# Performance work log

Hardware: AMD Instinct MI355X
Metric: run time of the kernel (lower is better)

Reference implementation:

```python
import jax, jax.numpy as jnp
import numpy as np

B, S, D, H, L, FF, V, TYPES = 16, 512, 1024, 16, 8, 4096, 30522, 2
DH = D // H
BETA = 1.0          # pbit_temperature
EPS = 1e-12         # layer_norm_eps
STD = 0.02          # initializer_range


def _ln(x, g, b):
    m = x.mean(-1, keepdims=True)
    v = ((x - m) ** 2).mean(-1, keepdims=True)
    return (x - m) * jax.lax.rsqrt(v + EPS) * g + b


def setup_inputs() -> dict:
    key = jax.random.key(0)
    ks = iter(jax.random.split(key, 32))
    rn = lambda shape: (jax.random.normal(next(ks), shape, dtype=jnp.float32) * STD)
    inp = {
        'input_ids': jax.random.randint(next(ks), (B, S), 0, V),
        'token_type_ids': jax.random.randint(next(ks), (B, S), 0, TYPES),
        'tok_emb': rn((V, D)),
        'pos_emb': rn((S, D)),
        'type_emb': rn((TYPES, D)),
        'emb_g': jnp.ones((D,), jnp.float32),
        'emb_b': jnp.zeros((D,), jnp.float32),
        # stacked per-layer parameters [L, ...]
        'Wq': rn((L, D, D)), 'bq': jnp.zeros((L, D), jnp.float32),
        'Wk': rn((L, D, D)), 'bk': jnp.zeros((L, D), jnp.float32),
        'Wv': rn((L, D, D)), 'bv': jnp.zeros((L, D), jnp.float32),
        'Wo': rn((L, D, D)), 'bo': jnp.zeros((L, D), jnp.float32),
        'ln1_g': jnp.ones((L, D), jnp.float32), 'ln1_b': jnp.zeros((L, D), jnp.float32),
        'ln2_g': jnp.ones((L, D), jnp.float32), 'ln2_b': jnp.zeros((L, D), jnp.float32),
        'W1': rn((L, D, FF)), 'b1': jnp.zeros((L, FF), jnp.float32),
        'W2': rn((L, FF, D)), 'b2': jnp.zeros((L, D), jnp.float32),
    }
    return inp


def reference(input_ids, token_type_ids, tok_emb, pos_emb, type_emb, emb_g, emb_b,
              Wq, bq, Wk, bk, Wv, bv, Wo, bo, ln1_g, ln1_b, ln2_g, ln2_b,
              W1, b1, W2, b2):
    # Embeddings (eval mode: TSU noise + dropout are identity)
    h = tok_emb[input_ids] + pos_emb[None, :, :] + type_emb[token_type_ids]
    h = _ln(h, emb_g, emb_b)

    def layer(h, p):
        wq, bq_, wk, bk_, wv, bv_, wo, bo_, g1, bb1, g2, bb2, w1, bf1, w2, bf2 = p
        x = _ln(h, g1, bb1)  # pre-LN per TinyBioBERTLayer
        q = (x @ wq + bq_).reshape(B, S, H, DH)
        k = (x @ wk + bk_).reshape(B, S, H, DH)
        v = (x @ wv + bv_).reshape(B, S, H, DH)
        # P-bit attention in expectation == temperature-scaled softmax SDPA
        scores = jnp.einsum('bqhd,bkhd->bhqk', q, k) * (BETA / np.sqrt(DH))
        a = jax.nn.softmax(scores, axis=-1)
        ctx = jnp.einsum('bhqk,bkhd->bqhd', a, v).reshape(B, S, D)
        h = h + ctx @ wo + bo_
        y = _ln(h, g2, bb2)
        y = jax.nn.gelu(y @ w1 + bf1, approximate=False) @ w2 + bf2
        return h + y, None

    params = (Wq, bq, Wk, bk, Wv, bv, Wo, bo, ln1_g, ln1_b, ln2_g, ln2_b, W1, b1, W2, b2)
    h, _ = jax.lax.scan(layer, h, params)
    return h
```

## Files before the change

### kernel.cpp

```cpp
#include <hip/hip_runtime.h>
#include <math.h>

#define B_  16
#define S_  512
#define D_  1024
#define H_  16
#define DH_ 64
#define L_  8
#define FF_ 4096
#define M_  (B_*S_)

typedef __attribute__((ext_vector_type(4))) float  f32x4;
typedef __attribute__((ext_vector_type(8))) short  s8v;
typedef __attribute__((ext_vector_type(4))) short  s4v;
typedef __attribute__((ext_vector_type(8))) __bf16 bf8v;

__device__ __forceinline__ short f2bf(float f) {
  union { float f; unsigned u; } x; x.f = f;
  unsigned r = x.u + 0x7fffu + ((x.u >> 16) & 1u);
  return (short)(r >> 16);
}

__device__ __forceinline__ f32x4 mfma16(s8v a, s8v b, f32x4 c) {
  return __builtin_amdgcn_mfma_f32_16x16x32_bf16(
      __builtin_bit_cast(bf8v, a), __builtin_bit_cast(bf8v, b), c, 0, 0, 0);
}

__device__ __forceinline__ float gelu_exact(float v) {
  return 0.5f * v * (1.0f + erff(v * 0.70710678118654752f));
}

__global__ __launch_bounds__(256) void tcvt(const float* __restrict__ src,
                                            short* __restrict__ dst, int R, int C) {
  __shared__ float tile[32][33];
  const size_t lo = (size_t)blockIdx.z * R * C;
  src += lo; dst += lo;
  const int c0 = blockIdx.x * 32, r0 = blockIdx.y * 32;
  const int tx = threadIdx.x & 31, ty = threadIdx.x >> 5;
#pragma unroll
  for (int i = 0; i < 32; i += 8)
    tile[ty + i][tx] = src[(size_t)(r0 + ty + i) * C + (c0 + tx)];
  __syncthreads();
#pragma unroll
  for (int i = 0; i < 32; i += 8)
    dst[(size_t)(c0 + ty + i) * R + (r0 + tx)] = f2bf(tile[tx][ty + i]);
}

__global__ __launch_bounds__(256) void embed_ln(
    const int* __restrict__ ids, const int* __restrict__ tts,
    const float* __restrict__ tok, const float* __restrict__ pos,
    const float* __restrict__ typ, const float* __restrict__ g,
    const float* __restrict__ bta, float* __restrict__ h) {
  const int row = blockIdx.x;
  const int s = row & (S_ - 1);
  const int id = ids[row], tt = tts[row];
  const int t = threadIdx.x;
  const float4 a = ((const float4*)(tok + (size_t)id * D_))[t];
  const float4 p = ((const float4*)(pos + (size_t)s  * D_))[t];
  const float4 y = ((const float4*)(typ + (size_t)tt * D_))[t];
  float x0 = a.x + p.x + y.x, x1 = a.y + p.y + y.y;
  float x2 = a.z + p.z + y.z, x3 = a.w + p.w + y.w;
  float sum = x0 + x1 + x2 + x3;
  float sq  = x0*x0 + x1*x1 + x2*x2 + x3*x3;
  __shared__ float red[8];
#pragma unroll
  for (int d = 1; d < 64; d <<= 1) { sum += __shfl_xor(sum, d); sq += __shfl_xor(sq, d); }
  if ((t & 63) == 0) { red[t >> 6] = sum; red[(t >> 6) + 4] = sq; }
  __syncthreads();
  sum = red[0] + red[1] + red[2] + red[3];
  sq  = red[4] + red[5] + red[6] + red[7];
  const float mean = sum * (1.f / D_);
  const float var  = sq * (1.f / D_) - mean * mean;
  const float rstd = rsqrtf(fmaxf(var, 0.f) + 1e-12f);
  const float4 gg = ((const float4*)g)[t];
  const float4 bb = ((const float4*)bta)[t];
  float4 o;
  o.x = (x0 - mean) * rstd * gg.x + bb.x;
  o.y = (x1 - mean) * rstd * gg.y + bb.y;
  o.z = (x2 - mean) * rstd * gg.z + bb.z;
  o.w = (x3 - mean) * rstd * gg.w + bb.w;
  ((float4*)(h + (size_t)row * D_))[t] = o;
}

__global__ __launch_bounds__(256) void ln_bf16(
    const float* __restrict__ h, const float* __restrict__ g,
    const float* __restrict__ bta, short* __restrict__ out) {
  const int row = blockIdx.x;
  const int t = threadIdx.x;
  const float4 x = ((const float4*)(h + (size_t)row * D_))[t];
  float sum = x.x + x.y + x.z + x.w;
  float sq  = x.x*x.x + x.y*x.y + x.z*x.z + x.w*x.w;
  __shared__ float red[8];
#pragma unroll
  for (int d = 1; d < 64; d <<= 1) { sum += __shfl_xor(sum, d); sq += __shfl_xor(sq, d); }
  if ((t & 63) == 0) { red[t >> 6] = sum; red[(t >> 6) + 4] = sq; }
  __syncthreads();
  sum = red[0] + red[1] + red[2] + red[3];
  sq  = red[4] + red[5] + red[6] + red[7];
  const float mean = sum * (1.f / D_);
  const float var  = sq * (1.f / D_) - mean * mean;
  const float rstd = rsqrtf(fmaxf(var, 0.f) + 1e-12f);
  const float4 gg = ((const float4*)g)[t];
  const float4 bb = ((const float4*)bta)[t];
  s4v o;
  o[0] = f2bf((x.x - mean) * rstd * gg.x + bb.x);
  o[1] = f2bf((x.y - mean) * rstd * gg.y + bb.y);
  o[2] = f2bf((x.z - mean) * rstd * gg.z + bb.z);
  o[3] = f2bf((x.w - mean) * rstd * gg.w + bb.w);
  *(s4v*)&out[(size_t)row * D_ + t * 4] = o;
}

template<int MODE>
__global__ __launch_bounds__(256, 2) void gemm_bt(
    const short* __restrict__ A, const short* __restrict__ Bt,
    const float* __restrict__ bias, short* __restrict__ out,
    float* __restrict__ hres, int N, int K) {
  __shared__ __align__(16) short As[128 * 32];
  __shared__ __align__(16) short Bs[128 * 32];
  const int tid = threadIdx.x;
  const int wid = tid >> 6, lane = tid & 63;
  const int wr = wid >> 1, wc = wid & 1;
  const int l15 = lane & 15, l4 = lane >> 4;

  const short* Ab = A + (size_t)blockIdx.x * 128 * K;
  const short* Bb = Bt + (size_t)blockIdx.y * 128 * K;

  const f32x4 zero4 = {0.f, 0.f, 0.f, 0.f};
  f32x4 acc[4][4];
#pragma unroll
  for (int i = 0; i < 4; ++i)
#pragma unroll
    for (int j = 0; j < 4; ++j) acc[i][j] = zero4;

  const int ldrow = wid * 32 + (lane >> 2);
  const int ldcol = (lane & 3) * 8;

  s8v ga[2], gb[2];
#pragma unroll
  for (int c = 0; c < 2; ++c) {
    ga[c] = *(const s8v*)(Ab + (size_t)(ldrow + c * 16) * K + ldcol);
    gb[c] = *(const s8v*)(Bb + (size_t)(ldrow + c * 16) * K + ldcol);
  }

  for (int k0 = 0; k0 < K; k0 += 32) {
#pragma unroll
    for (int c = 0; c < 2; ++c) {
      *(s8v*)&As[(ldrow + c * 16) * 32 + ldcol] = ga[c];
      *(s8v*)&Bs[(ldrow + c * 16) * 32 + ldcol] = gb[c];
    }
    __syncthreads();
    if (k0 + 32 < K) {
#pragma unroll
      for (int c = 0; c < 2; ++c) {
        ga[c] = *(const s8v*)(Ab + (size_t)(ldrow + c * 16) * K + (k0 + 32) + ldcol);
        gb[c] = *(const s8v*)(Bb + (size_t)(ldrow + c * 16) * K + (k0 + 32) + ldcol);
      }
    }
    s8v af[4], bf[4];
#pragma unroll
    for (int mf = 0; mf < 4; ++mf)
      af[mf] = *(const s8v*)&As[(wr * 64 + mf * 16 + l15) * 32 + l4 * 8];
#pragma unroll
    for (int nf = 0; nf < 4; ++nf)
      bf[nf] = *(const s8v*)&Bs[(wc * 64 + nf * 16 + l15) * 32 + l4 * 8];
#pragma unroll
    for (int mf = 0; mf < 4; ++mf)
#pragma unroll
      for (int nf = 0; nf < 4; ++nf)
        acc[mf][nf] = mfma16(af[mf], bf[nf], acc[mf][nf]);
    __syncthreads();
  }

  const int r0 = blockIdx.x * 128 + wr * 64;
  const int c0 = blockIdx.y * 128 + wc * 64;
#pragma unroll
  for (int mf = 0; mf < 4; ++mf) {
#pragma unroll
    for (int nf = 0; nf < 4; ++nf) {
      const int col = c0 + nf * 16 + l15;
      const float bb = bias[col];
#pragma unroll
      for (int r = 0; r < 4; ++r) {
        const int row = r0 + mf * 16 + l4 * 4 + r;
        const float v = acc[mf][nf][r] + bb;
        if (MODE == 0) {
          out[(size_t)row * N + col] = f2bf(v);
        } else if (MODE == 1) {
          out[(size_t)row * N + col] = f2bf(gelu_exact(v));
        } else if (MODE == 2) {
          hres[(size_t)row * N + col] += v;
        } else {
          const int b = row >> 9, s = row & 511, hd = col >> 6, dh = col & 63;
          out[((((size_t)b * H_ + hd) * S_ + s) << 6) + dh] = f2bf(v);
        }
      }
    }
  }
}

__global__ __launch_bounds__(256, 2) void attn(
    const short* __restrict__ Q, const short* __restrict__ K,
    const short* __restrict__ V, short* __restrict__ ctx) {
  __shared__ __align__(16) short Kl[32][72];
  __shared__ __align__(16) short Vt[DH_][40];
  __shared__ __align__(16) short Pl[4][32 * 40];

  const int tid = threadIdx.x, wid = tid >> 6, lane = tid & 63;
  const int l15 = lane & 15, l4 = lane >> 4;
  const int bh = blockIdx.y;
  const size_t base = (size_t)bh * S_ * DH_;
  const short* Qb = Q + base;
  const short* Kb = K + base;
  const short* Vb = V + base;

  const int qoff = blockIdx.x * 128 + wid * 32;

  s8v qf[2][2];
#pragma unroll
  for (int mf = 0; mf < 2; ++mf)
#pragma unroll
    for (int ks = 0; ks < 2; ++ks)
      qf[mf][ks] = *(const s8v*)&Qb[(size_t)(qoff + mf * 16 + l15) * DH_ + ks * 32 + l4 * 8];

  const f32x4 zero4 = {0.f, 0.f, 0.f, 0.f};
  f32x4 o[2][4];
  float rm[2][4], rs[2][4];
#pragma unroll
  for (int mf = 0; mf < 2; ++mf) {
#pragma unroll
    for (int nf = 0; nf < 4; ++nf) o[mf][nf] = zero4;
#pragma unroll
    for (int r = 0; r < 4; ++r) { rm[mf][r] = -1e30f; rs[mf][r] = 0.f; }
  }

  const int str = tid >> 3;
  const int stc = (tid & 7) * 8;

  for (int kt = 0; kt < S_ / 32; ++kt) {
    __syncthreads();
    {
      const s8v kk = *(const s8v*)&Kb[(size_t)(kt * 32 + str) * DH_ + stc];
      *(s8v*)&Kl[str][stc] = kk;
      const s8v vv = *(const s8v*)&Vb[(size_t)(kt * 32 + str) * DH_ + stc];
#pragma unroll
      for (int j = 0; j < 8; ++j) Vt[stc + j][str] = vv[j];
    }
    __syncthreads();

    f32x4 sc[2][2];
#pragma unroll
    for (int mf = 0; mf < 2; ++mf)
#pragma unroll
      for (int nt = 0; nt < 2; ++nt) sc[mf][nt] = zero4;
#pragma unroll
    for (int nt = 0; nt < 2; ++nt)
#pragma unroll
      for (int ks = 0; ks < 2; ++ks) {
        const s8v kf = *(const s8v*)&Kl[nt * 16 + l15][ks * 32 + l4 * 8];
#pragma unroll
        for (int mf = 0; mf < 2; ++mf)
          sc[mf][nt] = mfma16(qf[mf][ks], kf, sc[mf][nt]);
      }

#pragma unroll
    for (int mf = 0; mf < 2; ++mf) {
      float tm[4];
#pragma unroll
      for (int r = 0; r < 4; ++r) {
        sc[mf][0][r] *= 0.125f; sc[mf][1][r] *= 0.125f;
        tm[r] = fmaxf(sc[mf][0][r], sc[mf][1][r]);
      }
#pragma unroll
      for (int d = 1; d < 16; d <<= 1)
#pragma unroll
        for (int r = 0; r < 4; ++r) tm[r] = fmaxf(tm[r], __shfl_xor(tm[r], d));
      float ps[4];
#pragma unroll
      for (int r = 0; r < 4; ++r) {
        const float nm = fmaxf(rm[mf][r], tm[r]);
        const float so = __expf(rm[mf][r] - nm);
        rm[mf][r] = nm;
        rs[mf][r] *= so;
#pragma unroll
        for (int nf = 0; nf < 4; ++nf) o[mf][nf][r] *= so;
        const float p0 = __expf(sc[mf][0][r] - nm);
        const float p1 = __expf(sc[mf][1][r] - nm);
        sc[mf][0][r] = p0; sc[mf][1][r] = p1;
        ps[r] = p0 + p1;
      }
#pragma unroll
      for (int d = 1; d < 16; d <<= 1)
#pragma unroll
        for (int r = 0; r < 4; ++r) ps[r] += __shfl_xor(ps[r], d);
#pragma unroll
      for (int r = 0; r < 4; ++r) rs[mf][r] += ps[r];
#pragma unroll
      for (int nt = 0; nt < 2; ++nt)
#pragma unroll
        for (int r = 0; r < 4; ++r)
          Pl[wid][(mf * 16 + l4 * 4 + r) * 40 + nt * 16 + l15] = f2bf(sc[mf][nt][r]);
    }
    asm volatile("s_waitcnt lgkmcnt(0)" ::: "memory");

    s8v vf[4];
#pragma unroll
    for (int nf = 0; nf < 4; ++nf)
      vf[nf] = *(const s8v*)&Vt[nf * 16 + l15][l4 * 8];
#pragma unroll
    for (int mf = 0; mf < 2; ++mf) {
      const s8v pf = *(const s8v*)&Pl[wid][(mf * 16 + l15) * 40 + l4 * 8];
#pragma unroll
      for (int nf = 0; nf < 4; ++nf)
        o[mf][nf] = mfma16(pf, vf[nf], o[mf][nf]);
    }
  }

  const int bb = bh >> 4, hh = bh & 15;
#pragma unroll
  for (int mf = 0; mf < 2; ++mf)
#pragma unroll
    for (int r = 0; r < 4; ++r) {
      const int qrow = qoff + mf * 16 + l4 * 4 + r;
      const float inv = 1.0f / rs[mf][r];
      short* dst = ctx + (size_t)(bb * S_ + qrow) * D_ + hh * DH_;
#pragma unroll
      for (int nf = 0; nf < 4; ++nf)
        dst[nf * 16 + l15] = f2bf(o[mf][nf][r] * inv);
    }
}

extern "C" void kernel_launch(void* const* d_in, const int* in_sizes, int n_in,
                              void* d_out, int out_size, void* d_ws, size_t ws_size,
                              hipStream_t stream) {
  const int*   ids = (const int*)d_in[0];
  const int*   tts = (const int*)d_in[1];
  const float* tok = (const float*)d_in[2];
  const float* pos = (const float*)d_in[3];
  const float* typ = (const float*)d_in[4];
  const float* eg  = (const float*)d_in[5];
  const float* eb  = (const float*)d_in[6];
  const float* Wq  = (const float*)d_in[7];  const float* bq = (const float*)d_in[8];
  const float* Wk  = (const float*)d_in[9];  const float* bk = (const float*)d_in[10];
  const float* Wv  = (const float*)d_in[11]; const float* bv = (const float*)d_in[12];
  const float* Wo  = (const float*)d_in[13]; const float* bo = (const float*)d_in[14];
  const float* g1  = (const float*)d_in[15]; const float* be1 = (const float*)d_in[16];
  const float* g2  = (const float*)d_in[17]; const float* be2 = (const float*)d_in[18];
  const float* W1  = (const float*)d_in[19]; const float* b1 = (const float*)d_in[20];
  const float* W2  = (const float*)d_in[21]; const float* b2 = (const float*)d_in[22];

  float* h = (float*)d_out;

  const size_t szDD  = (size_t)D_ * D_ * 2;
  const size_t szDF  = (size_t)D_ * FF_ * 2;
  const size_t xb_b  = (size_t)M_ * D_ * 2;
  const size_t big_b = (size_t)M_ * FF_ * 2;
  const size_t wfull = (szDD * 4 + szDF * 2) * L_;
  const bool full = ws_size >= wfull + xb_b + big_b + 8192;

  char* p = (char*)d_ws;
  auto alloc = [&](size_t bytes) { char* r = p; p += (bytes + 255) & ~(size_t)255; return r; };
  const size_t wl = full ? L_ : 1;
  short* wqT = (short*)alloc(szDD * wl);
  short* wkT = (short*)alloc(szDD * wl);
  short* wvT = (short*)alloc(szDD * wl);
  short* woT = (short*)alloc(szDD * wl);
  short* w1T = (short*)alloc(szDF * wl);
  short* w2T = (short*)alloc(szDF * wl);
  short* xb  = (short*)alloc(xb_b);
  char*  big = alloc(big_b);
  short* qb  = (short*)big;
  short* kb  = (short*)(big + xb_b);
  short* vb  = (short*)(big + 2 * xb_b);
  short* cb  = xb;
  short* tb  = (short*)big;

  if (full) {
    tcvt<<<dim3(D_/32,  D_/32,  L_), 256, 0, stream>>>(Wq, wqT, D_,  D_);
    tcvt<<<dim3(D_/32,  D_/32,  L_), 256, 0, stream>>>(Wk, wkT, D_,  D_);
    tcvt<<<dim3(D_/32,  D_/32,  L_), 256, 0, stream>>>(Wv, wvT, D_,  D_);
    tcvt<<<dim3(D_/32,  D_/32,  L_), 256, 0, stream>>>(Wo, woT, D_,  D_);
    tcvt<<<dim3(FF_/32, D_/32,  L_), 256, 0, stream>>>(W1, w1T, D_,  FF_);
    tcvt<<<dim3(D_/32,  FF_/32, L_), 256, 0, stream>>>(W2, w2T, FF_, D_);
  }

  embed_ln<<<M_, 256, 0, stream>>>(ids, tts, tok, pos, typ, eg, eb, h);

  for (int l = 0; l < L_; ++l) {
    if (!full) {
      tcvt<<<dim3(D_/32,  D_/32,  1), 256, 0, stream>>>(Wq + (size_t)l*D_*D_,  wqT, D_,  D_);
      tcvt<<<dim3(D_/32,  D_/32,  1), 256, 0, stream>>>(Wk + (size_t)l*D_*D_,  wkT, D_,  D_);
      tcvt<<<dim3(D_/32,  D_/32,  1), 256, 0, stream>>>(Wv + (size_t)l*D_*D_,  wvT, D_,  D_);
      tcvt<<<dim3(D_/32,  D_/32,  1), 256, 0, stream>>>(Wo + (size_t)l*D_*D_,  woT, D_,  D_);
      tcvt<<<dim3(FF_/32, D_/32,  1), 256, 0, stream>>>(W1 + (size_t)l*D_*FF_, w1T, D_,  FF_);
      tcvt<<<dim3(D_/32,  FF_/32, 1), 256, 0, stream>>>(W2 + (size_t)l*D_*FF_, w2T, FF_, D_);
    }
    const size_t od = full ? (size_t)l * D_ * D_  : 0;
    const size_t of = full ? (size_t)l * D_ * FF_ : 0;

    ln_bf16<<<M_, 256, 0, stream>>>(h, g1 + l*D_, be1 + l*D_, xb);
    gemm_bt<3><<<dim3(M_/128, D_/128), 256, 0, stream>>>(xb, wqT + od, bq + l*D_, qb, nullptr, D_, D_);
    gemm_bt<3><<<dim3(M_/128, D_/128), 256, 0, stream>>>(xb, wkT + od, bk + l*D_, kb, nullptr, D_, D_);
    gemm_bt<3><<<dim3(M_/128, D_/128), 256, 0, stream>>>(xb, wvT + od, bv + l*D_, vb, nullptr, D_, D_);
    attn<<<dim3(S_/128, B_*H_), 256, 0, stream>>>(qb, kb, vb, cb);
    gemm_bt<2><<<dim3(M_/128, D_/128), 256, 0, stream>>>(cb, woT + od, bo + l*D_, nullptr, h, D_, D_);
    ln_bf16<<<M_, 256, 0, stream>>>(h, g2 + l*D_, be2 + l*D_, xb);
    gemm_bt<1><<<dim3(M_/128, FF_/128), 256, 0, stream>>>(xb, w1T + of, b1 + l*FF_, tb, nullptr, FF_, D_);
    gemm_bt<2><<<dim3(M_/128, D_/128), 256, 0, stream>>>(tb, w2T + of, b2 + l*D_, nullptr, h, D_, FF_);
  }
}
```

Baseline: 3.625 ms.

## Fuse QKV projections into one GEMM and load tiles via global_load_lds

The Q, K and V weights are packed into one concatenated transposed buffer, so a single GEMM launch with three times the N-dimension produces all three projections, choosing bias and output slab per column block. Separately, the GEMM main loop now uses direct global-to-LDS 16-byte loads in place of register staging with software prefetch. This cuts launches and reuses the A tiles across a wider grid, but the new loop drops the overlap of the next tile's loads with the current MFMAs, which may expose memory latency.

New measurement: 3.746 ms. 1.03x slower.

```diff
diff --git a/kernel.cpp b/kernel.cpp
--- a/kernel.cpp
+++ b/kernel.cpp
@@ -26,15 +26,22 @@
       __builtin_bit_cast(bf8v, a), __builtin_bit_cast(bf8v, b), c, 0, 0, 0);
 }
 
+__device__ __forceinline__ void gl_lds16(const void* g, void* lds) {
+  __builtin_amdgcn_global_load_lds(
+      (const __attribute__((address_space(1))) unsigned int*)g,
+      (__attribute__((address_space(3))) unsigned int*)lds, 16, 0, 0);
+}
+
 __device__ __forceinline__ float gelu_exact(float v) {
   return 0.5f * v * (1.0f + erff(v * 0.70710678118654752f));
 }
 
 __global__ __launch_bounds__(256) void tcvt(const float* __restrict__ src,
-                                            short* __restrict__ dst, int R, int C) {
+                                            short* __restrict__ dst, int R, int C,
+                                            size_t dls) {
   __shared__ float tile[32][33];
-  const size_t lo = (size_t)blockIdx.z * R * C;
-  src += lo; dst += lo;
+  src += (size_t)blockIdx.z * R * C;
+  dst += (size_t)blockIdx.z * dls;
   const int c0 = blockIdx.x * 32, r0 = blockIdx.y * 32;
   const int tx = threadIdx.x & 31, ty = threadIdx.x >> 5;
 #pragma unroll
@@ -113,7 +120,8 @@
 template<int MODE>
 __global__ __launch_bounds__(256, 2) void gemm_bt(
     const short* __restrict__ A, const short* __restrict__ Bt,
-    const float* __restrict__ bias, short* __restrict__ out,
+    const float* __restrict__ b0, const float* __restrict__ b1,
+    const float* __restrict__ b2, short* __restrict__ out,
     float* __restrict__ hres, int N, int K) {
   __shared__ __align__(16) short As[128 * 32];
   __shared__ __align__(16) short Bs[128 * 32];
@@ -132,30 +140,17 @@
 #pragma unroll
     for (int j = 0; j < 4; ++j) acc[i][j] = zero4;
 
-  const int ldrow = wid * 32 + (lane >> 2);
+  const int ldrow = lane >> 2;
   const int ldcol = (lane & 3) * 8;
 
-  s8v ga[2], gb[2];
-#pragma unroll
-  for (int c = 0; c < 2; ++c) {
-    ga[c] = *(const s8v*)(Ab + (size_t)(ldrow + c * 16) * K + ldcol);
-    gb[c] = *(const s8v*)(Bb + (size_t)(ldrow + c * 16) * K + ldcol);
-  }
-
   for (int k0 = 0; k0 < K; k0 += 32) {
 #pragma unroll
     for (int c = 0; c < 2; ++c) {
-      *(s8v*)&As[(ldrow + c * 16) * 32 + ldcol] = ga[c];
-      *(s8v*)&Bs[(ldrow + c * 16) * 32 + ldcol] = gb[c];
+      const int seg = wid * 2 + c;
+      gl_lds16(Ab + (size_t)(seg * 16 + ldrow) * K + (k0 + ldcol), (char*)As + seg * 1024);
+      gl_lds16(Bb + (size_t)(seg * 16 + ldrow) * K + (k0 + ldcol), (char*)Bs + seg * 1024);
     }
     __syncthreads();
-    if (k0 + 32 < K) {
-#pragma unroll
-      for (int c = 0; c < 2; ++c) {
-        ga[c] = *(const s8v*)(Ab + (size_t)(ldrow + c * 16) * K + (k0 + 32) + ldcol);
-        gb[c] = *(const s8v*)(Bb + (size_t)(ldrow + c * 16) * K + (k0 + 32) + ldcol);
-      }
-    }
     s8v af[4], bf[4];
 #pragma unroll
     for (int mf = 0; mf < 4; ++mf)
@@ -173,12 +168,17 @@
 
   const int r0 = blockIdx.x * 128 + wr * 64;
   const int c0 = blockIdx.y * 128 + wc * 64;
+  const int which = c0 >> 10;
+  const float* bias = (MODE == 3) ? (which == 0 ? b0 : (which == 1 ? b1 : b2)) : b0;
+  short* out3 = (MODE == 3) ? out + (size_t)which * M_ * D_ : out;
+
 #pragma unroll
   for (int mf = 0; mf < 4; ++mf) {
 #pragma unroll
     for (int nf = 0; nf < 4; ++nf) {
       const int col = c0 + nf * 16 + l15;
-      const float bb = bias[col];
+      const int colw = col & (D_ - 1);
+      const float bb = bias[MODE == 3 ? colw : col];
 #pragma unroll
       for (int r = 0; r < 4; ++r) {
         const int row = r0 + mf * 16 + l4 * 4 + r;
@@ -190,8 +190,8 @@
         } else if (MODE == 2) {
           hres[(size_t)row * N + col] += v;
         } else {
-          const int b = row >> 9, s = row & 511, hd = col >> 6, dh = col & 63;
-          out[((((size_t)b * H_ + hd) * S_ + s) << 6) + dh] = f2bf(v);
+          const int b = row >> 9, s = row & 511, hd = colw >> 6, dh = colw & 63;
+          out3[((((size_t)b * H_ + hd) * S_ + s) << 6) + dh] = f2bf(v);
         }
       }
     }
@@ -350,61 +350,60 @@
 
   float* h = (float*)d_out;
 
-  const size_t szDD  = (size_t)D_ * D_ * 2;
-  const size_t szDF  = (size_t)D_ * FF_ * 2;
+  const size_t szDD  = (size_t)D_ * D_;
+  const size_t szDF  = (size_t)D_ * FF_;
   const size_t xb_b  = (size_t)M_ * D_ * 2;
   const size_t big_b = (size_t)M_ * FF_ * 2;
-  const size_t wfull = (szDD * 4 + szDF * 2) * L_;
+  const size_t wfull = (szDD * 4 + szDF * 2) * 2 * L_;
   const bool full = ws_size >= wfull + xb_b + big_b + 8192;
 
   char* p = (char*)d_ws;
   auto alloc = [&](size_t bytes) { char* r = p; p += (bytes + 255) & ~(size_t)255; return r; };
   const size_t wl = full ? L_ : 1;
-  short* wqT = (short*)alloc(szDD * wl);
-  short* wkT = (short*)alloc(szDD * wl);
-  short* wvT = (short*)alloc(szDD * wl);
-  short* woT = (short*)alloc(szDD * wl);
-  short* w1T = (short*)alloc(szDF * wl);
-  short* w2T = (short*)alloc(szDF * wl);
+  short* wqkvT = (short*)alloc(szDD * 3 * 2 * wl);
+  short* woT   = (short*)alloc(szDD * 2 * wl);
+  short* w1T   = (short*)alloc(szDF * 2 * wl);
+  short* w2T   = (short*)alloc(szDF * 2 * wl);
   short* xb  = (short*)alloc(xb_b);
   char*  big = alloc(big_b);
   short* qb  = (short*)big;
-  short* kb  = (short*)(big + xb_b);
-  short* vb  = (short*)(big + 2 * xb_b);
   short* cb  = xb;
   short* tb  = (short*)big;
 
   if (full) {
-    tcvt<<<dim3(D_/32,  D_/32,  L_), 256, 0, stream>>>(Wq, wqT, D_,  D_);
-    tcvt<<<dim3(D_/32,  D_/32,  L_), 256, 0, stream>>>(Wk, wkT, D_,  D_);
-    tcvt<<<dim3(D_/32,  D_/32,  L_), 256, 0, stream>>>(Wv, wvT, D_,  D_);
-    tcvt<<<dim3(D_/32,  D_/32,  L_), 256, 0, stream>>>(Wo, woT, D_,  D_);
-    tcvt<<<dim3(FF_/32, D_/32,  L_), 256, 0, stream>>>(W1, w1T, D_,  FF_);
-    tcvt<<<dim3(D_/32,  FF_/32, L_), 256, 0, stream>>>(W2, w2T, FF_, D_);
+    tcvt<<<dim3(D_/32,  D_/32,  L_), 256, 0, stream>>>(Wq, wqkvT,            D_,  D_,  3*szDD);
+    tcvt<<<dim3(D_/32,  D_/32,  L_), 256, 0, stream>>>(Wk, wqkvT +   szDD,   D_,  D_,  3*szDD);
+    tcvt<<<dim3(D_/32,  D_/32,  L_), 256, 0, stream>>>(Wv, wqkvT + 2*szDD,   D_,  D_,  3*szDD);
+    tcvt<<<dim3(D_/32,  D_/32,  L_), 256, 0, stream>>>(Wo, woT, D_,  D_,  szDD);
+    tcvt<<<dim3(FF_/32, D_/32,  L_), 256, 0, stream>>>(W1, w1T, D_,  FF_, szDF);
+    tcvt<<<dim3(D_/32,  FF_/32, L_), 256, 0, stream>>>(W2, w2T, FF_, D_,  szDF);
   }
 
   embed_ln<<<M_, 256, 0, stream>>>(ids, tts, tok, pos, typ, eg, eb, h);
 
   for (int l = 0; l < L_; ++l) {
     if (!full) {
-      tcvt<<<dim3(D_/32,  D_/32,  1), 256, 0, stream>>>(Wq + (size_t)l*D_*D_,  wqT, D_,  D_);
-      tcvt<<<dim3(D_/32,  D_/32,  1), 256, 0, stream>>>(Wk + (size_t)l*D_*D_,  wkT, D_,  D_);
-      tcvt<<<dim3(D_/32,  D_/32,  1), 256, 0, stream>>>(Wv + (size_t)l*D_*D_,  wvT, D_,  D_);
-      tcvt<<<dim3(D_/32,  D_/32,  1), 256, 0, stream>>>(Wo + (size_t)l*D_*D_,  woT, D_,  D_);
-      tcvt<<<dim3(FF_/32, D_/32,  1), 256, 0, stream>>>(W1 + (size_t)l*D_*FF_, w1T, D_,  FF_);
-      tcvt<<<dim3(D_/32,  FF_/32, 1), 256, 0, stream>>>(W2 + (size_t)l*D_*FF_, w2T, FF_, D_);
-    }
-    const size_t od = full ? (size_t)l * D_ * D_  : 0;
-    const size_t of = full ? (size_t)l * D_ * FF_ : 0;
+      tcvt<<<dim3(D_/32,  D_/32,  1), 256, 0, stream>>>(Wq + (size_t)l*szDD, wqkvT,          D_,  D_,  0);
+      tcvt<<<dim3(D_/32,  D_/32,  1), 256, 0, stream>>>(Wk + (size_t)l*szDD, wqkvT +   szDD, D_,  D_,  0);
+      tcvt<<<dim3(D_/32,  D_/32,  1), 256, 0, stream>>>(Wv + (size_t)l*szDD, wqkvT + 2*szDD, D_,  D_,  0);
+      tcvt<<<dim3(D_/32,  D_/32,  1), 256, 0, stream>>>(Wo + (size_t)l*szDD, woT, D_,  D_,  0);
+      tcvt<<<dim3(FF_/32, D_/32,  1), 256, 0, stream>>>(W1 + (size_t)l*szDF, w1T, D_,  FF_, 0);
+      tcvt<<<dim3(D_/32,  FF_/32, 1), 256, 0, stream>>>(W2 + (size_t)l*szDF, w2T, FF_, D_,  0);
+    }
+    const size_t o3 = full ? (size_t)l * 3 * szDD : 0;
+    const size_t od = full ? (size_t)l * szDD : 0;
+    const size_t of = full ? (size_t)l * szDF : 0;
 
     ln_bf16<<<M_, 256, 0, stream>>>(h, g1 + l*D_, be1 + l*D_, xb);
-    gemm_bt<3><<<dim3(M_/128, D_/128), 256, 0, stream>>>(xb, wqT + od, bq + l*D_, qb, nullptr, D_, D_);
-    gemm_bt<3><<<dim3(M_/128, D_/128), 256, 0, stream>>>(xb, wkT + od, bk + l*D_, kb, nullptr, D_, D_);
-    gemm_bt<3><<<dim3(M_/128, D_/128), 256, 0, stream>>>(xb, wvT + od, bv + l*D_, vb, nullptr, D_, D_);
-    attn<<<dim3(S_/128, B_*H_), 256, 0, stream>>>(qb, kb, vb, cb);
-    gemm_bt<2><<<dim3(M_/128, D_/128), 256, 0, stream>>>(cb, woT + od, bo + l*D_, nullptr, h, D_, D_);
+    gemm_bt<3><<<dim3(M_/128, 3*D_/128), 256, 0, stream>>>(
+        xb, wqkvT + o3, bq + l*D_, bk + l*D_, bv + l*D_, qb, nullptr, D_, D_);
+    attn<<<dim3(S_/128, B_*H_), 256, 0, stream>>>(qb, qb + (size_t)M_*D_, qb + 2*(size_t)M_*D_, cb);
+    gemm_bt<2><<<dim3(M_/128, D_/128), 256, 0, stream>>>(
+        cb, woT + od, bo + l*D_, nullptr, nullptr, nullptr, h, D_, D_);
     ln_bf16<<<M_, 256, 0, stream>>>(h, g2 + l*D_, be2 + l*D_, xb);
-    gemm_bt<1><<<dim3(M_/128, FF_/128), 256, 0, stream>>>(xb, w1T + of, b1 + l*FF_, tb, nullptr, FF_, D_);
-    gemm_bt<2><<<dim3(M_/128, D_/128), 256, 0, stream>>>(tb, w2T + of, b2 + l*D_, nullptr, h, D_, FF_);
-  }
-}
+    gemm_bt<1><<<dim3(M_/128, FF_/128), 256, 0, stream>>>(
+        xb, w1T + of, b1 + l*FF_, nullptr, nullptr, tb, nullptr, FF_, D_);
+    gemm_bt<2><<<dim3(M_/128, D_/128), 256, 0, stream>>>(
+        tb, w2T + of, b2 + l*D_, nullptr, nullptr, nullptr, h, D_, FF_);
+  }
+}
```
